# Kernel tuning notes

Hardware: AMD Instinct MI355X
Metric: run time of the kernel (lower is better)

Reference implementation:

```python
import jax, jax.numpy as jnp
import numpy as np

B, F, V, D = 4096, 24, 1000, 32
RED = 8            # max(1, F // 3) SENet bottleneck
COMB = 2 * F * D   # 1536
EPS = 1e-5


def setup_inputs() -> dict:
    key = jax.random.key(0)
    ks = jax.random.split(key, 12)
    return {
        "x": jax.random.randint(ks[0], (B, F), 0, V),
        "emb_tables": jax.random.normal(ks[1], (F, V, D), jnp.float32) * 0.05,
        "lin_tables": jax.random.normal(ks[2], (F, V), jnp.float32) * 0.05,
        "bias": jnp.zeros((1,), jnp.float32),
        "se_w1": jax.random.normal(ks[3], (RED, F), jnp.float32) * 0.2,
        "se_w2": jax.random.normal(ks[4], (F, RED), jnp.float32) * 0.2,
        "bil_W": jax.random.normal(ks[5], (F, F, D, D), jnp.float32) * (1.0 / np.sqrt(D)),
        "w0": jax.random.normal(ks[6], (COMB, 1024), jnp.float32) * 0.02,
        "b0": jnp.zeros((1024,), jnp.float32),
        "g0": jnp.ones((1024,), jnp.float32),
        "be0": jnp.zeros((1024,), jnp.float32),
        "w1": jax.random.normal(ks[7], (1024, 512), jnp.float32) * 0.02,
        "b1": jnp.zeros((512,), jnp.float32),
        "g1": jnp.ones((512,), jnp.float32),
        "be1": jnp.zeros((512,), jnp.float32),
        "w2": jax.random.normal(ks[8], (512, 1), jnp.float32) * 0.02,
        "b2": jnp.zeros((1,), jnp.float32),
    }


def _bilinear_field_interaction(e, W):
    # e: [B,F,D], W: [F,F,D,D]
    # out[b,i,k] = e[b,i,k] * sum_{j != i} (W[i,j] @ e[b,j])[k]
    t = jnp.einsum('ijkl,bjl->bijk', W, e)          # [B,F,F,D]
    mask = 1.0 - jnp.eye(F, dtype=e.dtype)          # zero the i==j terms
    s = jnp.einsum('bijk,ij->bik', t, mask)         # [B,F,D]
    return e * s


def _senet(e, w1, w2):
    Z = e.mean(axis=2)                              # [B,F] squeeze
    A = jax.nn.sigmoid(jax.nn.relu(Z @ w1.T) @ w2.T)  # [B,F]
    return e * A[:, :, None]


def _bn_train(h, g, b):
    m = h.mean(axis=0)
    v = h.var(axis=0)  # biased, matches torch BN normalization
    return g * (h - m) * jax.lax.rsqrt(v + EPS) + b


def reference(x, emb_tables, lin_tables, bias, se_w1, se_w2, bil_W,
              w0, b0, g0, be0, w1, b1, g1, be1, w2, b2):
    fidx = jnp.arange(F)[None, :]                   # [1,F]
    emb = emb_tables[fidx, x]                       # [B,F,D]
    lin = lin_tables[fidx, x].sum(axis=1)           # [B] first-order term

    se_emb = _senet(emb, se_w1, se_w2)
    p = _bilinear_field_interaction(emb, bil_W)     # [B,F,D]
    q = _bilinear_field_interaction(se_emb, bil_W)  # [B,F,D]
    combined = jnp.concatenate(
        [p.reshape(B, F * D), q.reshape(B, F * D)], axis=1)  # [B,2FD]

    h = jax.nn.relu(_bn_train(combined @ w0 + b0, g0, be0))
    h = jax.nn.relu(_bn_train(h @ w1 + b1, g1, be1))
    mlp_out = (h @ w2 + b2)[:, 0]                   # [B]

    logit = lin + bias[0] + mlp_out
    return jax.nn.sigmoid(logit)                    # [B]
```

## Files before the change

### kernel.cpp

```cpp
#include <hip/hip_runtime.h>

#define B_SZ 4096
#define F_SZ 24
#define V_SZ 1000
#define D_SZ 32
#define RED  8
#define FD   768
#define COMB 1536
#define H0   1024
#define H1   512
#define EPS  1e-5f

typedef __bf16 bf16x8 __attribute__((ext_vector_type(8)));
typedef float  f32x4  __attribute__((ext_vector_type(4)));
typedef const __attribute__((address_space(1))) unsigned int* gptr_t;
typedef       __attribute__((address_space(3))) unsigned int* lptr_t;

__device__ __forceinline__ float bf2f(unsigned short u) {
    union { unsigned int i; float f; } v; v.i = ((unsigned int)u) << 16; return v.f;
}
__device__ __forceinline__ unsigned short f2bf(float f) {
    union { float f; unsigned int i; } v; v.f = f;
    unsigned int u = v.i;
    return (unsigned short)((u + 0x7FFFu + ((u >> 16) & 1u)) >> 16);
}
__device__ __forceinline__ unsigned int pack2(float a, float b) {
    return (unsigned int)f2bf(a) | ((unsigned int)f2bf(b) << 16);
}

__global__ __launch_bounds__(256) void prep_gather(
        const int* __restrict__ x, const float* __restrict__ emb,
        const float* __restrict__ lint, const float* __restrict__ sw1,
        const float* __restrict__ sw2, const float* __restrict__ bw,
        unsigned short* __restrict__ Xbf, unsigned short* __restrict__ Wt,
        float* __restrict__ lin, float* __restrict__ sums) {
    int bid = blockIdx.x;
    int tid = threadIdx.x;
    if (bid < 1024) {
        int w = tid >> 6, lane = tid & 63;
        int b = bid * 4 + w;
        __shared__ int   xi[4][F_SZ];
        __shared__ float e[4][F_SZ][D_SZ];
        __shared__ float Z[4][F_SZ];
        __shared__ float r1[4][RED];
        __shared__ float Afac[4][F_SZ];
        if (lane < F_SZ) xi[w][lane] = x[b * F_SZ + lane];
        __syncthreads();
        #pragma unroll
        for (int it = 0; it < 3; it++) {
            int idx = it * 64 + lane;
            int f = idx >> 3, k4 = (idx & 7) * 4;
            float4 v = *(const float4*)&emb[((size_t)f * V_SZ + xi[w][f]) * D_SZ + k4];
            *(float4*)&e[w][f][k4] = v;
        }
        __syncthreads();
        if (lane < F_SZ) {
            float s = 0.f;
            #pragma unroll
            for (int k = 0; k < D_SZ; k++) s += e[w][lane][k];
            Z[w][lane] = s * (1.f / D_SZ);
        }
        __syncthreads();
        if (lane < RED) {
            float s = 0.f;
            #pragma unroll
            for (int f = 0; f < F_SZ; f++) s += Z[w][f] * sw1[lane * F_SZ + f];
            r1[w][lane] = fmaxf(s, 0.f);
        }
        __syncthreads();
        if (lane < F_SZ) {
            float s = 0.f;
            #pragma unroll
            for (int r = 0; r < RED; r++) s += r1[w][r] * sw2[lane * RED + r];
            Afac[w][lane] = 1.f / (1.f + expf(-s));
        }
        __syncthreads();
        #pragma unroll
        for (int it = 0; it < 3; it++) {
            int idx = it * 64 + lane;
            int f = idx >> 3, k4 = (idx & 7) * 4;
            const float* p = &e[w][f][k4];
            uint2 u, us;
            u.x = pack2(p[0], p[1]); u.y = pack2(p[2], p[3]);
            float a = Afac[w][f];
            us.x = pack2(p[0] * a, p[1] * a); us.y = pack2(p[2] * a, p[3] * a);
            *(uint2*)&Xbf[(size_t)b * FD + idx * 4] = u;
            *(uint2*)&Xbf[(size_t)(B_SZ + b) * FD + idx * 4] = us;
        }
        float lv = (lane < F_SZ) ? lint[lane * V_SZ + xi[w][lane]] : 0.f;
        #pragma unroll
        for (int off = 32; off > 0; off >>= 1) lv += __shfl_down(lv, off);
        if (lane == 0) lin[b] = lv;
    } else if (bid < 3328) {
        int o = (bid - 1024) * 256 + tid;
        int ik = o / FD, jl = o - ik * FD;
        int i = ik >> 5, k = ik & 31, j = jl >> 5, l = jl & 31;
        Wt[o] = (i == j) ? (unsigned short)0
                         : f2bf(bw[(((size_t)i * F_SZ + j) * D_SZ + k) * D_SZ + l]);
    } else {
        int o = (bid - 3328) * 256 + tid;
        sums[o] = 0.f;
    }
}

template<int MODE, int K, int N, int TM, int TN, int GX, int GY>
__global__ __launch_bounds__(256) void mfma_gemm(
        const unsigned short* __restrict__ A,
        const unsigned short* __restrict__ Bt,
        const float* __restrict__ bias,
        const unsigned short* __restrict__ Xbf,
        unsigned short* __restrict__ Obf,
        float* __restrict__ sum, float* __restrict__ sumsq,
        const float* __restrict__ psum, const float* __restrict__ psumsq,
        const float* __restrict__ g, const float* __restrict__ be,
        const float* __restrict__ tw0, const float* __restrict__ tw1,
        unsigned short* __restrict__ tw0t, unsigned short* __restrict__ tw1t) {
    constexpr int MI = TM / 32, NI = TN / 32;
    constexpr int NSUB = 4;
    constexpr int CLD = TN + 4;
    constexpr int STAGE = (TM + TN) * 256;
    constexpr int CST   = TM * CLD * 4;
    constexpr int SMEM  = STAGE > CST ? STAGE : CST;
    __shared__ __align__(16) char smem[SMEM];
    unsigned short* Abuf = (unsigned short*)smem;
    unsigned short* Bbuf = (unsigned short*)(smem + TM * 256);
    float* Cst = (float*)smem;
    __shared__ float sc_s[MODE == 2 ? K : 1];
    __shared__ float sh_s[MODE == 2 ? K : 1];
    const int tid  = threadIdx.x;
    const int bid = blockIdx.x;

    if (MODE == 0 && bid >= GX * GY) {
        int t = bid - GX * GY;
        const float* in; unsigned short* out; int Kt, Nt, bx, by;
        if (t < 1536) { in = tw0; out = tw0t; Kt = COMB; Nt = H0; bx = t & 31; by = t >> 5; }
        else { t -= 1536; in = tw1; out = tw1t; Kt = H0; Nt = H1; bx = t & 15; by = t >> 4; }
        float (*tile)[33] = (float(*)[33])smem;
        int tx = tid & 31, ty = tid >> 5;
        int n0 = bx * 32, k0t = by * 32;
        #pragma unroll
        for (int r = 0; r < 32; r += 8)
            tile[ty + r][tx] = in[(size_t)(k0t + ty + r) * Nt + n0 + tx];
        __syncthreads();
        #pragma unroll
        for (int r = 0; r < 32; r += 8)
            out[(size_t)(n0 + ty + r) * Kt + k0t + tx] = f2bf(tile[tx][ty + r]);
        return;
    }

    const int lane = tid & 63, wv = tid >> 6;
    const int wm = (wv >> 1) * (TM / 2), wn = (wv & 1) * (TN / 2);
    const int fr = lane & 15, kq = lane >> 4;
    const int xcd = bid & 7, slot = bid >> 3;
    const int rowb = xcd * (GY / 8) + slot / GX;
    const int colb = slot % GX;
    const int bm = rowb * TM, bn = colb * TN;
    const int srow = tid >> 2;
    const int skc  = (tid & 3) * 8;

    if (MODE == 2) {
        #pragma unroll
        for (int q = 0; q < K / 256; q++) {
            int c = q * 256 + tid;
            float m = psum[c] * (1.f / B_SZ);
            float var = psumsq[c] * (1.f / B_SZ) - m * m;
            float rstd = rsqrtf(var + EPS);
            float sc = g[c] * rstd;
            sc_s[c] = sc;
            sh_s[c] = be[c] - m * sc;
        }
        __syncthreads();
    }

    f32x4 acc[MI][NI];
    #pragma unroll
    for (int i = 0; i < MI; i++)
        #pragma unroll
        for (int j = 0; j < NI; j++) {
            f32x4 z = {0.f, 0.f, 0.f, 0.f};
            acc[i][j] = z;
        }

    uint4 hvA[NSUB];
    if (MODE == 2) {
        #pragma unroll
        for (int s = 0; s < NSUB; s++)
            hvA[s] = *(const uint4*)&A[(size_t)(bm + srow) * K + 32 * s + skc];
    }

    for (int k0 = 0; k0 < K; k0 += 32 * NSUB) {
        if (MODE == 2) {
            #pragma unroll
            for (int s = 0; s < NSUB; s++) {
                unsigned int uu[4] = {hvA[s].x, hvA[s].y, hvA[s].z, hvA[s].w};
                unsigned int oo[4];
                #pragma unroll
                for (int q = 0; q < 4; q++) {
                    int c = k0 + 32 * s + skc + 2 * q;
                    float v0 = bf2f((unsigned short)(uu[q] & 0xFFFF)) * sc_s[c] + sh_s[c];
                    float v1 = bf2f((unsigned short)(uu[q] >> 16)) * sc_s[c + 1] + sh_s[c + 1];
                    oo[q] = pack2(fmaxf(v0, 0.f), fmaxf(v1, 0.f));
                }
                uint4 ov; ov.x = oo[0]; ov.y = oo[1]; ov.z = oo[2]; ov.w = oo[3];
                *(uint4*)&Abuf[s * TM * 32 + srow * 32 + skc] = ov;
            }
            if (k0 + 32 * NSUB < K) {
                #pragma unroll
                for (int s = 0; s < NSUB; s++)
                    hvA[s] = *(const uint4*)&A[(size_t)(bm + srow) * K + k0 + 32 * NSUB + 32 * s + skc];
            }
        } else {
            #pragma unroll
            for (int s = 0; s < NSUB; s++)
                #pragma unroll
                for (int c = 0; c < TM / 64; c++) {
                    const unsigned short* ga = A + (size_t)(bm + c * 64 + srow) * K + k0 + 32 * s + skc;
                    char* la = smem + s * TM * 64 + c * 4096 + wv * 1024;
                    __builtin_amdgcn_global_load_lds((gptr_t)ga, (lptr_t)la, 16, 0, 0);
                }
        }
        #pragma unroll
        for (int s = 0; s < NSUB; s++)
            #pragma unroll
            for (int c = 0; c < TN / 64; c++) {
                const unsigned short* gb = Bt + (size_t)(bn + c * 64 + srow) * K + k0 + 32 * s + skc;
                char* lb = smem + TM * 256 + s * TN * 64 + c * 4096 + wv * 1024;
                __builtin_amdgcn_global_load_lds((gptr_t)gb, (lptr_t)lb, 16, 0, 0);
            }
        __syncthreads();
        #pragma unroll
        for (int s = 0; s < NSUB; s++) {
            bf16x8 af[MI], bfv[NI];
            #pragma unroll
            for (int mi = 0; mi < MI; mi++)
                af[mi] = *(const bf16x8*)&Abuf[s * TM * 32 + (wm + mi * 16 + fr) * 32 + kq * 8];
            #pragma unroll
            for (int ni = 0; ni < NI; ni++)
                bfv[ni] = *(const bf16x8*)&Bbuf[s * TN * 32 + (wn + ni * 16 + fr) * 32 + kq * 8];
            #pragma unroll
            for (int mi = 0; mi < MI; mi++)
                #pragma unroll
                for (int ni = 0; ni < NI; ni++)
                    acc[mi][ni] = __builtin_amdgcn_mfma_f32_16x16x32_bf16(
                        af[mi], bfv[ni], acc[mi][ni], 0, 0, 0);
        }
        __syncthreads();
    }

    if (MODE != 0) {
        #pragma unroll
        for (int ni = 0; ni < NI; ni++) {
            int col = bn + wn + ni * 16 + fr;
            float bv = bias[col];
            float s = 0.f, ss = 0.f;
            #pragma unroll
            for (int mi = 0; mi < MI; mi++)
                #pragma unroll
                for (int r = 0; r < 4; r++) {
                    float v = acc[mi][ni][r] + bv;
                    acc[mi][ni][r] = v;
                    s += v; ss += v * v;
                }
            s  += __shfl_xor(s, 16);  s  += __shfl_xor(s, 32);
            ss += __shfl_xor(ss, 16); ss += __shfl_xor(ss, 32);
            if (kq == 0) {
                atomicAdd(&sum[col], s);
                atomicAdd(&sumsq[col], ss);
            }
        }
    }

    #pragma unroll
    for (int mi = 0; mi < MI; mi++)
        #pragma unroll
        for (int ni = 0; ni < NI; ni++) {
            int lrow = wm + mi * 16 + kq * 4;
            int lcol = wn + ni * 16 + fr;
            #pragma unroll
            for (int r = 0; r < 4; r++)
                Cst[(lrow + r) * CLD + lcol] = acc[mi][ni][r];
        }
    __syncthreads();
    #pragma unroll
    for (int ps = 0; ps < TM / 32; ps++) {
        int rl = ps * 32 + (tid >> 3);
        int cl = (tid & 7) * 8;
        float4 va = *(const float4*)&Cst[rl * CLD + cl];
        float4 vb = *(const float4*)&Cst[rl * CLD + cl + 4];
        float v[8] = {va.x, va.y, va.z, va.w, vb.x, vb.y, vb.z, vb.w};
        int grow = bm + rl, gcol = bn + cl;
        if (MODE == 0) {
            uint4 xv = *(const uint4*)&Xbf[(size_t)grow * FD + gcol];
            unsigned int xu[4] = {xv.x, xv.y, xv.z, xv.w};
            unsigned int oo[4];
            #pragma unroll
            for (int q = 0; q < 4; q++) {
                float x0 = bf2f((unsigned short)(xu[q] & 0xFFFF));
                float x1 = bf2f((unsigned short)(xu[q] >> 16));
                oo[q] = pack2(x0 * v[2 * q], x1 * v[2 * q + 1]);
            }
            uint4 ov; ov.x = oo[0]; ov.y = oo[1]; ov.z = oo[2]; ov.w = oo[3];
            size_t off = (grow < B_SZ)
                ? ((size_t)grow * COMB + gcol)
                : ((size_t)(grow - B_SZ) * COMB + FD + gcol);
            *(uint4*)&Obf[off] = ov;
        } else {
            unsigned int oo[4];
            #pragma unroll
            for (int q = 0; q < 4; q++)
                oo[q] = pack2(v[2 * q], v[2 * q + 1]);
            uint4 ov; ov.x = oo[0]; ov.y = oo[1]; ov.z = oo[2]; ov.w = oo[3];
            *(uint4*)&Obf[(size_t)grow * N + gcol] = ov;
        }
    }
}

__global__ __launch_bounds__(256) void final_k(const unsigned short* __restrict__ h1,
        const float* __restrict__ sum, const float* __restrict__ sumsq,
        const float* __restrict__ g, const float* __restrict__ be,
        const float* __restrict__ w2, const float* __restrict__ b2,
        const float* __restrict__ lin, const float* __restrict__ bias,
        float* __restrict__ out) {
    __shared__ float sc_s[H1], sh_s[H1], w2_s[H1];
    int t = threadIdx.x;
    int wv = t >> 6, lane = t & 63;
    #pragma unroll
    for (int q = 0; q < 2; q++) {
        int c = q * 256 + t;
        float m = sum[c] * (1.f / B_SZ);
        float var = sumsq[c] * (1.f / B_SZ) - m * m;
        float rstd = rsqrtf(var + EPS);
        float sc = g[c] * rstd;
        sc_s[c] = sc;
        sh_s[c] = be[c] - m * sc;
        w2_s[c] = w2[c];
    }
    __syncthreads();
    int r0 = blockIdx.x * 16;
    #pragma unroll
    for (int i = 0; i < 4; i++) {
        int row = r0 + wv * 4 + i;
        int c0 = lane * 8;
        uint4 hv = *(const uint4*)&h1[(size_t)row * H1 + c0];
        unsigned int uu[4] = {hv.x, hv.y, hv.z, hv.w};
        float acc = 0.f;
        #pragma unroll
        for (int q = 0; q < 4; q++) {
            int c = c0 + 2 * q;
            float v0 = bf2f((unsigned short)(uu[q] & 0xFFFF)) * sc_s[c] + sh_s[c];
            float v1 = bf2f((unsigned short)(uu[q] >> 16)) * sc_s[c + 1] + sh_s[c + 1];
            acc += fmaxf(v0, 0.f) * w2_s[c] + fmaxf(v1, 0.f) * w2_s[c + 1];
        }
        #pragma unroll
        for (int off = 32; off > 0; off >>= 1) acc += __shfl_down(acc, off);
        if (lane == 0) {
            float logit = lin[row] + bias[0] + acc + b2[0];
            out[row] = 1.f / (1.f + expf(-logit));
        }
    }
}

extern "C" void kernel_launch(void* const* d_in, const int* in_sizes, int n_in,
                              void* d_out, int out_size, void* d_ws, size_t ws_size,
                              hipStream_t stream) {
    const int*   x    = (const int*)d_in[0];
    const float* emb  = (const float*)d_in[1];
    const float* lint = (const float*)d_in[2];
    const float* bias = (const float*)d_in[3];
    const float* sw1  = (const float*)d_in[4];
    const float* sw2  = (const float*)d_in[5];
    const float* bw   = (const float*)d_in[6];
    const float* w0   = (const float*)d_in[7];
    const float* b0   = (const float*)d_in[8];
    const float* g0   = (const float*)d_in[9];
    const float* be0  = (const float*)d_in[10];
    const float* w1   = (const float*)d_in[11];
    const float* b1   = (const float*)d_in[12];
    const float* g1   = (const float*)d_in[13];
    const float* be1  = (const float*)d_in[14];
    const float* w2   = (const float*)d_in[15];
    const float* b2   = (const float*)d_in[16];
    float* out = (float*)d_out;

    char* p = (char*)d_ws;
    auto alloc = [&](size_t bytes) { char* r = p; p += (bytes + 255) & ~(size_t)255; return r; };

    unsigned short* Xbf  = (unsigned short*)alloc((size_t)2 * B_SZ * FD * 2);
    unsigned short* Wt   = (unsigned short*)alloc((size_t)FD * FD * 2);
    unsigned short* w0t  = (unsigned short*)alloc((size_t)H0 * COMB * 2);
    unsigned short* w1t  = (unsigned short*)alloc((size_t)H1 * H0 * 2);
    unsigned short* Cbf  = (unsigned short*)alloc((size_t)B_SZ * COMB * 2);
    unsigned short* h0bf = (unsigned short*)alloc((size_t)B_SZ * H0 * 2);
    unsigned short* h1bf = (unsigned short*)alloc((size_t)B_SZ * H1 * 2);
    float* lin = (float*)alloc(B_SZ * 4);
    float* sums = (float*)alloc((2 * H0 + 2 * H1) * 4);
    float* sum0 = sums, *sumsq0 = sums + H0, *sum1 = sums + 2 * H0, *sumsq1 = sums + 2 * H0 + H1;

    prep_gather<<<3340, 256, 0, stream>>>(x, emb, lint, sw1, sw2, bw,
                                          Xbf, Wt, lin, sums);

    mfma_gemm<0, FD, FD, 128, 64, 12, 64><<<768 + 2048, 256, 0, stream>>>(
        Xbf, Wt, nullptr, Xbf, Cbf, nullptr, nullptr, nullptr, nullptr, nullptr, nullptr,
        w0, w1, w0t, w1t);
    mfma_gemm<1, COMB, H0, 64, 64, 16, 64><<<1024, 256, 0, stream>>>(
        Cbf, w0t, b0, nullptr, h0bf, sum0, sumsq0, nullptr, nullptr, nullptr, nullptr,
        nullptr, nullptr, nullptr, nullptr);
    mfma_gemm<2, H0, H1, 64, 64, 8, 64><<<512, 256, 0, stream>>>(
        h0bf, w1t, b1, nullptr, h1bf, sum1, sumsq1, sum0, sumsq0, g0, be0,
        nullptr, nullptr, nullptr, nullptr);
    final_k<<<B_SZ / 16, 256, 0, stream>>>(h1bf, sum1, sumsq1, g1, be1,
                                           w2, b2, lin, bias, out);
}
```

Measured before the change: 164.7 us.

## Fuse all stages into one persistent cooperative kernel with grid syncs

Result: slower. 428.7 us (+160.4%).

```diff
diff --git a/kernel.cpp b/kernel.cpp
--- a/kernel.cpp
+++ b/kernel.cpp
@@ -1,4 +1,6 @@
 #include <hip/hip_runtime.h>
+#include <hip/hip_cooperative_groups.h>
+namespace cg = cooperative_groups;
 
 #define B_SZ 4096
 #define F_SZ 24
@@ -28,83 +30,96 @@
     return (unsigned int)f2bf(a) | ((unsigned int)f2bf(b) << 16);
 }
 
-__global__ __launch_bounds__(256) void prep_gather(
+#define SMEM_BYTES 49152
+
+__device__ __forceinline__ void gather8(int bid, char* smem,
         const int* __restrict__ x, const float* __restrict__ emb,
         const float* __restrict__ lint, const float* __restrict__ sw1,
-        const float* __restrict__ sw2, const float* __restrict__ bw,
-        unsigned short* __restrict__ Xbf, unsigned short* __restrict__ Wt,
-        float* __restrict__ lin, float* __restrict__ sums) {
-    int bid = blockIdx.x;
+        const float* __restrict__ sw2,
+        unsigned short* __restrict__ Xbf, float* __restrict__ lin) {
     int tid = threadIdx.x;
-    if (bid < 1024) {
-        int w = tid >> 6, lane = tid & 63;
-        int b = bid * 4 + w;
-        __shared__ int   xi[4][F_SZ];
-        __shared__ float e[4][F_SZ][D_SZ];
-        __shared__ float Z[4][F_SZ];
-        __shared__ float r1[4][RED];
-        __shared__ float Afac[4][F_SZ];
-        if (lane < F_SZ) xi[w][lane] = x[b * F_SZ + lane];
+    int w = tid >> 6, lane = tid & 63;
+    int* xi   = (int*)smem;
+    float* e  = (float*)(smem + 512);
+    float* Z  = (float*)(smem + 13056);
+    float* r1 = (float*)(smem + 13568);
+    float* Af = (float*)(smem + 13824);
+    #pragma unroll
+    for (int r = 0; r < 2; r++) {
+        __syncthreads();
+        int b = bid * 8 + r * 4 + w;
+        if (lane < F_SZ) xi[w * F_SZ + lane] = x[b * F_SZ + lane];
         __syncthreads();
         #pragma unroll
         for (int it = 0; it < 3; it++) {
             int idx = it * 64 + lane;
             int f = idx >> 3, k4 = (idx & 7) * 4;
-            float4 v = *(const float4*)&emb[((size_t)f * V_SZ + xi[w][f]) * D_SZ + k4];
-            *(float4*)&e[w][f][k4] = v;
+            float4 v = *(const float4*)&emb[((size_t)f * V_SZ + xi[w * F_SZ + f]) * D_SZ + k4];
+            *(float4*)&e[(w * F_SZ + f) * D_SZ + k4] = v;
         }
         __syncthreads();
         if (lane < F_SZ) {
             float s = 0.f;
             #pragma unroll
-            for (int k = 0; k < D_SZ; k++) s += e[w][lane][k];
-            Z[w][lane] = s * (1.f / D_SZ);
+            for (int k = 0; k < D_SZ; k++) s += e[(w * F_SZ + lane) * D_SZ + k];
+            Z[w * F_SZ + lane] = s * (1.f / D_SZ);
         }
         __syncthreads();
         if (lane < RED) {
             float s = 0.f;
             #pragma unroll
-            for (int f = 0; f < F_SZ; f++) s += Z[w][f] * sw1[lane * F_SZ + f];
-            r1[w][lane] = fmaxf(s, 0.f);
+            for (int f = 0; f < F_SZ; f++) s += Z[w * F_SZ + f] * sw1[lane * F_SZ + f];
+            r1[w * RED + lane] = fmaxf(s, 0.f);
         }
         __syncthreads();
         if (lane < F_SZ) {
             float s = 0.f;
             #pragma unroll
-            for (int r = 0; r < RED; r++) s += r1[w][r] * sw2[lane * RED + r];
-            Afac[w][lane] = 1.f / (1.f + expf(-s));
+            for (int r2 = 0; r2 < RED; r2++) s += r1[w * RED + r2] * sw2[lane * RED + r2];
+            Af[w * F_SZ + lane] = 1.f / (1.f + expf(-s));
         }
         __syncthreads();
         #pragma unroll
         for (int it = 0; it < 3; it++) {
             int idx = it * 64 + lane;
             int f = idx >> 3, k4 = (idx & 7) * 4;
-            const float* p = &e[w][f][k4];
+            const float* p = &e[(w * F_SZ + f) * D_SZ + k4];
             uint2 u, us;
             u.x = pack2(p[0], p[1]); u.y = pack2(p[2], p[3]);
-            float a = Afac[w][f];
+            float a = Af[w * F_SZ + f];
             us.x = pack2(p[0] * a, p[1] * a); us.y = pack2(p[2] * a, p[3] * a);
             *(uint2*)&Xbf[(size_t)b * FD + idx * 4] = u;
             *(uint2*)&Xbf[(size_t)(B_SZ + b) * FD + idx * 4] = us;
         }
-        float lv = (lane < F_SZ) ? lint[lane * V_SZ + xi[w][lane]] : 0.f;
+        float lv = (lane < F_SZ) ? lint[lane * V_SZ + xi[w * F_SZ + lane]] : 0.f;
         #pragma unroll
         for (int off = 32; off > 0; off >>= 1) lv += __shfl_down(lv, off);
         if (lane == 0) lin[b] = lv;
-    } else if (bid < 3328) {
-        int o = (bid - 1024) * 256 + tid;
-        int ik = o / FD, jl = o - ik * FD;
-        int i = ik >> 5, k = ik & 31, j = jl >> 5, l = jl & 31;
-        Wt[o] = (i == j) ? (unsigned short)0
-                         : f2bf(bw[(((size_t)i * F_SZ + j) * D_SZ + k) * D_SZ + l]);
-    } else {
-        int o = (bid - 3328) * 256 + tid;
-        sums[o] = 0.f;
-    }
+    }
+}
+
+__device__ __forceinline__ void transpose_tile(int t, char* smem,
+        const float* __restrict__ w0, const float* __restrict__ w1,
+        unsigned short* __restrict__ w0t, unsigned short* __restrict__ w1t) {
+    __syncthreads();
+    const float* in; unsigned short* out; int Kt, Nt, bx, by;
+    if (t < 1536) { in = w0; out = w0t; Kt = COMB; Nt = H0; bx = t & 31; by = t >> 5; }
+    else { t -= 1536; in = w1; out = w1t; Kt = H0; Nt = H1; bx = t & 15; by = t >> 4; }
+    float (*tile)[33] = (float(*)[33])smem;
+    int tid = threadIdx.x;
+    int tx = tid & 31, ty = tid >> 5;
+    int n0 = bx * 32, k0t = by * 32;
+    #pragma unroll
+    for (int r = 0; r < 32; r += 8)
+        tile[ty + r][tx] = in[(size_t)(k0t + ty + r) * Nt + n0 + tx];
+    __syncthreads();
+    #pragma unroll
+    for (int r = 0; r < 32; r += 8)
+        out[(size_t)(n0 + ty + r) * Kt + k0t + tx] = f2bf(tile[tx][ty + r]);
 }
 
 template<int MODE, int K, int N, int TM, int TN, int GX, int GY>
-__global__ __launch_bounds__(256) void mfma_gemm(
+__device__ __forceinline__ void gemm_tile(int bid, char* smem,
         const unsigned short* __restrict__ A,
         const unsigned short* __restrict__ Bt,
         const float* __restrict__ bias,
@@ -112,42 +127,16 @@
         unsigned short* __restrict__ Obf,
         float* __restrict__ sum, float* __restrict__ sumsq,
         const float* __restrict__ psum, const float* __restrict__ psumsq,
-        const float* __restrict__ g, const float* __restrict__ be,
-        const float* __restrict__ tw0, const float* __restrict__ tw1,
-        unsigned short* __restrict__ tw0t, unsigned short* __restrict__ tw1t) {
+        const float* __restrict__ g, const float* __restrict__ be) {
     constexpr int MI = TM / 32, NI = TN / 32;
     constexpr int NSUB = 4;
     constexpr int CLD = TN + 4;
-    constexpr int STAGE = (TM + TN) * 256;
-    constexpr int CST   = TM * CLD * 4;
-    constexpr int SMEM  = STAGE > CST ? STAGE : CST;
-    __shared__ __align__(16) char smem[SMEM];
     unsigned short* Abuf = (unsigned short*)smem;
     unsigned short* Bbuf = (unsigned short*)(smem + TM * 256);
-    float* Cst = (float*)smem;
-    __shared__ float sc_s[MODE == 2 ? K : 1];
-    __shared__ float sh_s[MODE == 2 ? K : 1];
+    float* Cst  = (float*)smem;
+    float* sc_s = (float*)(smem + (TM + TN) * 256);
+    float* sh_s = sc_s + (MODE == 2 ? K : 0);
     const int tid  = threadIdx.x;
-    const int bid = blockIdx.x;
-
-    if (MODE == 0 && bid >= GX * GY) {
-        int t = bid - GX * GY;
-        const float* in; unsigned short* out; int Kt, Nt, bx, by;
-        if (t < 1536) { in = tw0; out = tw0t; Kt = COMB; Nt = H0; bx = t & 31; by = t >> 5; }
-        else { t -= 1536; in = tw1; out = tw1t; Kt = H0; Nt = H1; bx = t & 15; by = t >> 4; }
-        float (*tile)[33] = (float(*)[33])smem;
-        int tx = tid & 31, ty = tid >> 5;
-        int n0 = bx * 32, k0t = by * 32;
-        #pragma unroll
-        for (int r = 0; r < 32; r += 8)
-            tile[ty + r][tx] = in[(size_t)(k0t + ty + r) * Nt + n0 + tx];
-        __syncthreads();
-        #pragma unroll
-        for (int r = 0; r < 32; r += 8)
-            out[(size_t)(n0 + ty + r) * Kt + k0t + tx] = f2bf(tile[tx][ty + r]);
-        return;
-    }
-
     const int lane = tid & 63, wv = tid >> 6;
     const int wm = (wv >> 1) * (TM / 2), wn = (wv & 1) * (TN / 2);
     const int fr = lane & 15, kq = lane >> 4;
@@ -158,6 +147,7 @@
     const int srow = tid >> 2;
     const int skc  = (tid & 3) * 8;
 
+    __syncthreads();
     if (MODE == 2) {
         #pragma unroll
         for (int q = 0; q < K / 256; q++) {
@@ -315,15 +305,19 @@
     }
 }
 
-__global__ __launch_bounds__(256) void final_k(const unsigned short* __restrict__ h1,
+__device__ __forceinline__ void final_tile(int bid, char* smem,
+        const unsigned short* __restrict__ h1,
         const float* __restrict__ sum, const float* __restrict__ sumsq,
         const float* __restrict__ g, const float* __restrict__ be,
         const float* __restrict__ w2, const float* __restrict__ b2,
         const float* __restrict__ lin, const float* __restrict__ bias,
         float* __restrict__ out) {
-    __shared__ float sc_s[H1], sh_s[H1], w2_s[H1];
+    float* sc_s = (float*)smem;
+    float* sh_s = sc_s + H1;
+    float* w2_s = sh_s + H1;
     int t = threadIdx.x;
     int wv = t >> 6, lane = t & 63;
+    __syncthreads();
     #pragma unroll
     for (int q = 0; q < 2; q++) {
         int c = q * 256 + t;
@@ -336,7 +330,7 @@
         w2_s[c] = w2[c];
     }
     __syncthreads();
-    int r0 = blockIdx.x * 16;
+    int r0 = bid * 16;
     #pragma unroll
     for (int i = 0; i < 4; i++) {
         int row = r0 + wv * 4 + i;
@@ -358,6 +352,58 @@
             out[row] = 1.f / (1.f + expf(-logit));
         }
     }
+}
+
+__global__ __launch_bounds__(256, 2) void pers(
+        const int* x, const float* emb, const float* lint,
+        const float* sw1, const float* sw2, const float* bw,
+        const float* w0, const float* w1,
+        const float* b0, const float* g0, const float* be0,
+        const float* b1, const float* g1, const float* be1,
+        const float* w2, const float* b2, const float* bias,
+        unsigned short* Xbf, unsigned short* Wt,
+        unsigned short* w0t, unsigned short* w1t,
+        unsigned short* Cbf, unsigned short* h0bf, unsigned short* h1bf,
+        float* lin, float* sums, float* out) {
+    __shared__ __align__(16) char smem[SMEM_BYTES];
+    cg::grid_group grid = cg::this_grid();
+    const int bid = blockIdx.x;
+    const int tid = threadIdx.x;
+    const int gid = bid * 256 + tid;
+    float* sum0 = sums, *sumsq0 = sums + H0, *sum1 = sums + 2 * H0, *sumsq1 = sums + 2 * H0 + H1;
+
+    for (int o = gid; o < 2 * H0 + 2 * H1; o += 512 * 256) sums[o] = 0.f;
+    for (int o = gid; o < FD * FD; o += 512 * 256) {
+        int ik = o / FD, jl = o - ik * FD;
+        int i = ik >> 5, k = ik & 31, j = jl >> 5, l = jl & 31;
+        Wt[o] = (i == j) ? (unsigned short)0
+                         : f2bf(bw[(((size_t)i * F_SZ + j) * D_SZ + k) * D_SZ + l]);
+    }
+    gather8(bid, smem, x, emb, lint, sw1, sw2, Xbf, lin);
+    grid.sync();
+
+    gemm_tile<0, FD, FD, 128, 64, 12, 64>(bid, smem, Xbf, Wt, nullptr, Xbf, Cbf,
+        nullptr, nullptr, nullptr, nullptr, nullptr, nullptr);
+    if (bid < 256) {
+        gemm_tile<0, FD, FD, 128, 64, 12, 64>(512 + bid, smem, Xbf, Wt, nullptr, Xbf, Cbf,
+            nullptr, nullptr, nullptr, nullptr, nullptr, nullptr);
+    } else {
+        #pragma unroll
+        for (int i = 0; i < 8; i++)
+            transpose_tile((bid - 256) * 8 + i, smem, w0, w1, w0t, w1t);
+    }
+    grid.sync();
+
+    gemm_tile<1, COMB, H0, 128, 64, 16, 32>(bid, smem, Cbf, w0t, b0, nullptr, h0bf,
+        sum0, sumsq0, nullptr, nullptr, nullptr, nullptr);
+    grid.sync();
+
+    gemm_tile<2, H0, H1, 64, 64, 8, 64>(bid, smem, h0bf, w1t, b1, nullptr, h1bf,
+        sum1, sumsq1, sum0, sumsq0, g0, be0);
+    grid.sync();
+
+    if (bid < 256)
+        final_tile(bid, smem, h1bf, sum1, sumsq1, g1, be1, w2, b2, lin, bias, out);
 }
 
 extern "C" void kernel_launch(void* const* d_in, const int* in_sizes, int n_in,
@@ -392,22 +438,16 @@
     unsigned short* Cbf  = (unsigned short*)alloc((size_t)B_SZ * COMB * 2);
     unsigned short* h0bf = (unsigned short*)alloc((size_t)B_SZ * H0 * 2);
     unsigned short* h1bf = (unsigned short*)alloc((size_t)B_SZ * H1 * 2);
-    float* lin = (float*)alloc(B_SZ * 4);
+    float* lin  = (float*)alloc(B_SZ * 4);
     float* sums = (float*)alloc((2 * H0 + 2 * H1) * 4);
-    float* sum0 = sums, *sumsq0 = sums + H0, *sum1 = sums + 2 * H0, *sumsq1 = sums + 2 * H0 + H1;
-
-    prep_gather<<<3340, 256, 0, stream>>>(x, emb, lint, sw1, sw2, bw,
-                                          Xbf, Wt, lin, sums);
-
-    mfma_gemm<0, FD, FD, 128, 64, 12, 64><<<768 + 2048, 256, 0, stream>>>(
-        Xbf, Wt, nullptr, Xbf, Cbf, nullptr, nullptr, nullptr, nullptr, nullptr, nullptr,
-        w0, w1, w0t, w1t);
-    mfma_gemm<1, COMB, H0, 64, 64, 16, 64><<<1024, 256, 0, stream>>>(
-        Cbf, w0t, b0, nullptr, h0bf, sum0, sumsq0, nullptr, nullptr, nullptr, nullptr,
-        nullptr, nullptr, nullptr, nullptr);
-    mfma_gemm<2, H0, H1, 64, 64, 8, 64><<<512, 256, 0, stream>>>(
-        h0bf, w1t, b1, nullptr, h1bf, sum1, sumsq1, sum0, sumsq0, g0, be0,
-        nullptr, nullptr, nullptr, nullptr);
-    final_k<<<B_SZ / 16, 256, 0, stream>>>(h1bf, sum1, sumsq1, g1, be1,
-                                           w2, b2, lin, bias, out);
-}
+
+    void* args[] = {
+        (void*)&x, (void*)&emb, (void*)&lint, (void*)&sw1, (void*)&sw2, (void*)&bw,
+        (void*)&w0, (void*)&w1, (void*)&b0, (void*)&g0, (void*)&be0,
+        (void*)&b1, (void*)&g1, (void*)&be1, (void*)&w2, (void*)&b2, (void*)&bias,
+        (void*)&Xbf, (void*)&Wt, (void*)&w0t, (void*)&w1t,
+        (void*)&Cbf, (void*)&h0bf, (void*)&h1bf,
+        (void*)&lin, (void*)&sums, (void*)&out
+    };
+    hipLaunchCooperativeKernel((const void*)pers, dim3(512), dim3(256), args, 0, stream);
+}
```
